# Kernel tuning notes

Hardware: AMD Instinct MI355X
Metric: run time of the kernel (lower is better)

## Reference

```python
import jax, jax.numpy as jnp
import numpy as np

N_NODES = 100000
N_EDGES = 1600000
IN = 128
OUT = 32
HEADS = 4
NEG_SLOPE = 0.2


def setup_inputs() -> dict:
    key = jax.random.key(0)
    ks = jax.random.split(key, 6)
    x = jax.random.normal(ks[0], (N_NODES, IN), dtype=jnp.float32)
    row = jax.random.randint(ks[1], (N_EDGES,), 0, N_NODES, dtype=jnp.int32)
    col = jax.random.randint(ks[2], (N_EDGES,), 0, N_NODES, dtype=jnp.int32)
    W = jax.random.normal(ks[3], (OUT * HEADS, IN), dtype=jnp.float32) * (1.0 / np.sqrt(IN))
    b = jnp.zeros((OUT * HEADS,), dtype=jnp.float32)
    a_l = jax.random.normal(ks[4], (1, OUT, HEADS), dtype=jnp.float32) * 0.1
    a_r = jax.random.normal(ks[5], (1, OUT, HEADS), dtype=jnp.float32) * 0.1
    return {"x": x, "row": row, "col": col, "W": W, "b": b, "a_l": a_l, "a_r": a_r}


def reference(x, row, col, W, b, a_l, a_r):
    N = x.shape[0]
    # Z: [N, OUT, HEADS] (row-major view of [N, OUT*HEADS], matching torch .view)
    Z = (x @ W.T + b).reshape(N, OUT, HEADS)
    e_l = jnp.sum(Z * a_l, axis=1)  # [N, HEADS]
    e_r = jnp.sum(Z * a_r, axis=1)  # [N, HEADS]
    e = e_l[row] + e_r[col]         # [E, HEADS]
    e = jnp.where(e > 0, e, NEG_SLOPE * e)  # LeakyReLU
    # segment softmax over edges grouped by destination (row)
    m = jax.ops.segment_max(e, row, num_segments=N)      # [N, HEADS]
    ex = jnp.exp(e - m[row])                              # [E, HEADS]
    denom = jax.ops.segment_sum(ex, row, num_segments=N)  # [N, HEADS]
    alpha = ex / denom[row]                               # [E, HEADS]
    # bspmm: out[i,:,h] = sum_{(i,j) in E} alpha[e,h] * Z[j,:,h]
    out = jax.ops.segment_sum(alpha[:, None, :] * Z[col], row, num_segments=N)
    return out
```

## Files before the change

### kernel.cpp

```cpp
#include <hip/hip_runtime.h>
#include <hip/hip_bf16.h>
#include <math.h>


typedef __attribute__((ext_vector_type(8))) short bf16x8;
typedef __attribute__((ext_vector_type(4))) float f32x4;

__device__ __forceinline__ ushort f2bf(float f) {
  __hip_bfloat16 h = __float2bfloat16(f);
  return __builtin_bit_cast(ushort, h);
}
__device__ __forceinline__ float bf2f(ushort u) {
  unsigned v = ((unsigned)u) << 16;
  return __builtin_bit_cast(float, v);
}

__global__ __launch_bounds__(256, 2) void gemm_deg(
    const float* __restrict__ x, const float* __restrict__ W,
    const float* __restrict__ bias, ushort* __restrict__ Zh, int N,
    const int* __restrict__ row, int* __restrict__ deg,
    int* __restrict__ rank, int E, int G1) {
  __shared__ ushort xh[64 * 128];
  __shared__ ushort xl[64 * 128];

  if ((int)blockIdx.x >= G1) {
    int e = ((int)blockIdx.x - G1) * 256 + threadIdx.x;
    if (e < E) rank[e] = atomicAdd(&deg[row[e]], 1);
    return;
  }

  const int t = threadIdx.x;
  const int lane = t & 63;
  const int wv = t >> 6;
  const int row0 = blockIdx.x * 64;
  const int l15 = lane & 15, l4 = lane >> 4;

  bf16x8 Bh[2][4], Bl[2][4];
#pragma unroll
  for (int ct = 0; ct < 2; ++ct) {
    int ch = wv * 32 + ct * 16 + l15;
#pragma unroll
    for (int kf = 0; kf < 4; ++kf) {
      int k0 = kf * 32 + l4 * 8;
      const float* wp = W + (size_t)ch * 128 + k0;
      float4 w0 = *(const float4*)(wp);
      float4 w1 = *(const float4*)(wp + 4);
      float wf[8] = {w0.x, w0.y, w0.z, w0.w, w1.x, w1.y, w1.z, w1.w};
      bf16x8 hi, lo;
#pragma unroll
      for (int j = 0; j < 8; ++j) {
        ushort hb = f2bf(wf[j]);
        hi[j] = (short)hb;
        lo[j] = (short)f2bf(wf[j] - bf2f(hb));
      }
      Bh[ct][kf] = hi;
      Bl[ct][kf] = lo;
    }
  }

#pragma unroll
  for (int i = 0; i < 8; ++i) {
    int f4 = i * 256 + t;
    int r = f4 >> 5;
    int k = (f4 & 31) * 4;
    int gr = row0 + r;
    float4 v = make_float4(0.f, 0.f, 0.f, 0.f);
    if (gr < N) v = ((const float4*)x)[(size_t)gr * 32 + (f4 & 31)];
    float vf[4] = {v.x, v.y, v.z, v.w};
    ushort hs[4], ls[4];
#pragma unroll
    for (int j = 0; j < 4; ++j) {
      hs[j] = f2bf(vf[j]);
      ls[j] = f2bf(vf[j] - bf2f(hs[j]));
    }
    int idx = r * 128 + (k ^ ((r & 7) << 3));
    uint2 hv, lv;
    hv.x = hs[0] | ((unsigned)hs[1] << 16);
    hv.y = hs[2] | ((unsigned)hs[3] << 16);
    lv.x = ls[0] | ((unsigned)ls[1] << 16);
    lv.y = ls[2] | ((unsigned)ls[3] << 16);
    *(uint2*)&xh[idx] = hv;
    *(uint2*)&xl[idx] = lv;
  }
  __syncthreads();

  f32x4 acc[4][2];
#pragma unroll
  for (int rt = 0; rt < 4; ++rt)
#pragma unroll
    for (int ct = 0; ct < 2; ++ct) acc[rt][ct] = (f32x4){0.f, 0.f, 0.f, 0.f};

#pragma unroll
  for (int kf = 0; kf < 4; ++kf) {
#pragma unroll
    for (int rt = 0; rt < 4; ++rt) {
      int r = rt * 16 + l15;
      int k = kf * 32 + l4 * 8;
      int idx = r * 128 + (k ^ ((r & 7) << 3));
      bf16x8 ah = *(const bf16x8*)&xh[idx];
      bf16x8 al = *(const bf16x8*)&xl[idx];
#pragma unroll
      for (int ct = 0; ct < 2; ++ct) {
        acc[rt][ct] = __builtin_amdgcn_mfma_f32_16x16x32_bf16(ah, Bh[ct][kf], acc[rt][ct], 0, 0, 0);
        acc[rt][ct] = __builtin_amdgcn_mfma_f32_16x16x32_bf16(al, Bh[ct][kf], acc[rt][ct], 0, 0, 0);
        acc[rt][ct] = __builtin_amdgcn_mfma_f32_16x16x32_bf16(ah, Bl[ct][kf], acc[rt][ct], 0, 0, 0);
      }
    }
  }

  float bv[2];
  bv[0] = bias[wv * 32 + l15];
  bv[1] = bias[wv * 32 + 16 + l15];
#pragma unroll
  for (int rt = 0; rt < 4; ++rt) {
#pragma unroll
    for (int ct = 0; ct < 2; ++ct) {
      int ch = wv * 32 + ct * 16 + l15;
      unsigned zc = (unsigned)((ch & 3) * 32 + (ch >> 2));
#pragma unroll
      for (int j = 0; j < 4; ++j) {
        int r = row0 + rt * 16 + l4 * 4 + j;
        if (r < N) {
          float v = acc[rt][ct][j] + bv[ct];
          Zh[(unsigned)r * 128 + zc] = f2bf(v);
        }
      }
    }
  }
}

__global__ __launch_bounds__(256) void node_scan(
    const ushort* __restrict__ Zh, const float* __restrict__ a_l,
    const float* __restrict__ a_r, float* __restrict__ el,
    float* __restrict__ er, int N4,
    const int* __restrict__ deg, int* __restrict__ basev,
    int* __restrict__ bsum, int N, int G1) {
  __shared__ float sal[128], sar[128];
  __shared__ int ss[256];
  int t = threadIdx.x;

  if ((int)blockIdx.x < G1) {
    if (t < 128) { sal[t] = a_l[t]; sar[t] = a_r[t]; }
    __syncthreads();
    int idx = blockIdx.x * 256 + t;
    if (idx >= N4) return;
    int n = idx >> 2, h = idx & 3;
    const ushort* zp = Zh + (unsigned)n * 128 + h * 32;
    float sl = 0.f, sr = 0.f;
#pragma unroll
    for (int q = 0; q < 8; ++q) {
      uint2 zz = *(const uint2*)&zp[q * 4];
      float z0 = bf2f((ushort)(zz.x & 0xffff));
      float z1 = bf2f((ushort)(zz.x >> 16));
      float z2 = bf2f((ushort)(zz.y & 0xffff));
      float z3 = bf2f((ushort)(zz.y >> 16));
      int o = q * 4;
      sl += z0 * sal[(o + 0) * 4 + h] + z1 * sal[(o + 1) * 4 + h]
          + z2 * sal[(o + 2) * 4 + h] + z3 * sal[(o + 3) * 4 + h];
      sr += z0 * sar[(o + 0) * 4 + h] + z1 * sar[(o + 1) * 4 + h]
          + z2 * sar[(o + 2) * 4 + h] + z3 * sar[(o + 3) * 4 + h];
    }
    el[idx] = sl;
    er[idx] = sr;
  } else {
    int bid = (int)blockIdx.x - G1;
    int i = bid * 256 + t;
    int v = (i < N) ? deg[i] : 0;
    ss[t] = v;
    __syncthreads();
#pragma unroll
    for (int off = 1; off < 256; off <<= 1) {
      int u = (t >= off) ? ss[t - off] : 0;
      __syncthreads();
      ss[t] += u;
      __syncthreads();
    }
    if (i < N) basev[i] = ss[t] - v;
    if (t == 255) bsum[bid] = ss[255];
  }
}

__global__ __launch_bounds__(512) void scan2(int* __restrict__ bsum, int NB) {
  __shared__ int s[512];
  int v = (threadIdx.x < NB) ? bsum[threadIdx.x] : 0;
  s[threadIdx.x] = v;
  __syncthreads();
#pragma unroll
  for (int off = 1; off < 512; off <<= 1) {
    int t = (threadIdx.x >= off) ? s[threadIdx.x - off] : 0;
    __syncthreads();
    s[threadIdx.x] += t;
    __syncthreads();
  }
  if (threadIdx.x < NB) bsum[threadIdx.x] = s[threadIdx.x] - v;
}

__global__ __launch_bounds__(256) void fill(
    const int* __restrict__ row, const int* __restrict__ col,
    const int* __restrict__ rank, const int* __restrict__ base,
    const int* __restrict__ bsum, int* __restrict__ sorted_col, int E) {
  int e = blockIdx.x * 256 + threadIdx.x;
  if (e < E) {
    int r = row[e];
    sorted_col[base[r] + bsum[r >> 8] + rank[e]] = col[e];
  }
}

__global__ __launch_bounds__(256) void gather(
    const int* __restrict__ base, const int* __restrict__ bsum,
    const int* __restrict__ deg, const int* __restrict__ sorted_col,
    const float* __restrict__ el, const float* __restrict__ er,
    const ushort* __restrict__ Zh, float* __restrict__ out, int N) {
  int t = threadIdx.x;
  int lane = t & 63;
  int n = blockIdx.x * 4 + (t >> 6);
  if (n >= N) return;
  int h = lane >> 4;
  int j = lane & 15;
  int s = base[n] + bsum[n >> 8];
  int d = deg[n];
  int end = s + d;
  float elv = el[((unsigned)n << 2) + h];
  float acc0 = 0.f, acc1 = 0.f, sumA = 0.f;
  const unsigned* Zh32 = (const unsigned*)Zh;
  const unsigned zlane = (unsigned)lane;
  const int bpb = (lane & 48) << 2;

  for (int p = s; p < end; p += 16) {
    int cnt = end - p;
    int cl6 = 0;
    float xv = 0.f;
    if (j < cnt) {
      int cl = sorted_col[p + j];
      float e = elv + er[((unsigned)cl << 2) + h];
      e = fmaxf(e, 0.2f * e);
      xv = __expf(e);
      cl6 = cl << 6;
    }
    sumA += xv;
    float xvb[16];
    unsigned addr[16];
#pragma unroll
    for (int jj = 0; jj < 16; ++jj) {
      int a = bpb + (jj << 2);
      xvb[jj] = __builtin_bit_cast(float,
          __builtin_amdgcn_ds_bpermute(a, __builtin_bit_cast(int, xv)));
      addr[jj] = (unsigned)__builtin_amdgcn_ds_bpermute(a, cl6) + zlane;
    }
    unsigned zz[16];
#pragma unroll
    for (int jj = 0; jj < 16; ++jj) zz[jj] = Zh32[addr[jj]];
#pragma unroll
    for (int jj = 0; jj < 16; ++jj) {
      acc0 = fmaf(xvb[jj], __builtin_bit_cast(float, zz[jj] << 16), acc0);
      acc1 = fmaf(xvb[jj], __builtin_bit_cast(float, zz[jj] & 0xffff0000u), acc1);
    }
  }
  float sum = sumA;
  sum += __shfl_xor(sum, 1, 64);
  sum += __shfl_xor(sum, 2, 64);
  sum += __shfl_xor(sum, 4, 64);
  sum += __shfl_xor(sum, 8, 64);
  float inv = (d > 0) ? 1.0f / sum : 0.f;
  unsigned o0 = (unsigned)(j << 1);
  unsigned ob = ((unsigned)n << 7) + (o0 << 2) + (unsigned)h;
  out[ob] = acc0 * inv;
  out[ob + 4] = acc1 * inv;
}

extern "C" void kernel_launch(void* const* d_in, const int* in_sizes, int n_in,
                              void* d_out, int out_size, void* d_ws, size_t ws_size,
                              hipStream_t stream) {
  const float* x   = (const float*)d_in[0];
  const int*   row = (const int*)d_in[1];
  const int*   col = (const int*)d_in[2];
  const float* W   = (const float*)d_in[3];
  const float* b   = (const float*)d_in[4];
  const float* a_l = (const float*)d_in[5];
  const float* a_r = (const float*)d_in[6];
  float* out = (float*)d_out;

  const int N = in_sizes[0] / 128;
  const int E = in_sizes[1];
  const int NB = (N + 255) / 256;

  char* w = (char*)d_ws;
  ushort* Zh       = (ushort*)w;             w += (size_t)N * 128 * 2;
  int*   sorted_col= (int*)w;                w += (size_t)E * 4;
  int*   rank      = (int*)w;                w += (size_t)E * 4;
  float* el        = (float*)w;              w += (size_t)N * 4 * 4;
  float* er        = (float*)w;              w += (size_t)N * 4 * 4;
  int*   deg       = (int*)w;                w += (size_t)N * 4;
  int*   base      = (int*)w;                w += (size_t)N * 4;
  int*   bsum      = (int*)w;                w += 512 * 4;

  hipMemsetAsync(deg, 0, (size_t)N * sizeof(int), stream);

  const int G1g = (N + 63) / 64;
  const int G2d = (E + 255) / 256;
  gemm_deg<<<G1g + G2d, 256, 0, stream>>>(x, W, b, Zh, N, row, deg, rank, E, G1g);

  const int G1n = (N * 4 + 255) / 256;
  node_scan<<<G1n + NB, 256, 0, stream>>>(Zh, a_l, a_r, el, er, N * 4,
                                          deg, base, bsum, N, G1n);
  scan2<<<1, 512, 0, stream>>>(bsum, NB);
  fill<<<(E + 255) / 256, 256, 0, stream>>>(row, col, rank, base, bsum,
                                            sorted_col, E);
  gather<<<(N + 3) / 4, 256, 0, stream>>>(base, bsum, deg, sorted_col, el, er,
                                          Zh, out, N);
}
```

Before: 208.9 us.

## Split fused gemm/degree kernel, precompute bf16 weight splits, use 512-thread GEMM blocks

Precomputes the hi/lo bf16 split of W once in a small prep kernel instead of in every GEMM block. The degree-counting atomics move from the fused gemm_deg launch into their own kernel. The GEMM now runs 8 waves per block, each handling 16 output channels, so per-thread accumulator and B-fragment registers are halved and occupancy can rise. This adds two kernel launches and drops the overlap the fused launch gave between atomics and the GEMM.

```diff
diff --git a/kernel.cpp b/kernel.cpp
--- a/kernel.cpp
+++ b/kernel.cpp
@@ -15,52 +15,40 @@
   return __builtin_bit_cast(float, v);
 }
 
-__global__ __launch_bounds__(256, 2) void gemm_deg(
-    const float* __restrict__ x, const float* __restrict__ W,
-    const float* __restrict__ bias, ushort* __restrict__ Zh, int N,
-    const int* __restrict__ row, int* __restrict__ deg,
-    int* __restrict__ rank, int E, int G1) {
+__global__ __launch_bounds__(256) void prep_w(
+    const float* __restrict__ W, ushort* __restrict__ Wh,
+    ushort* __restrict__ Wl) {
+  int i = blockIdx.x * 256 + threadIdx.x;
+  float w = W[i];
+  ushort hb = f2bf(w);
+  Wh[i] = hb;
+  Wl[i] = f2bf(w - bf2f(hb));
+}
+
+__global__ __launch_bounds__(512, 4) void gemm_z(
+    const float* __restrict__ x, const ushort* __restrict__ Wh,
+    const ushort* __restrict__ Wl, const float* __restrict__ bias,
+    ushort* __restrict__ Zh, int N) {
   __shared__ ushort xh[64 * 128];
   __shared__ ushort xl[64 * 128];
-
-  if ((int)blockIdx.x >= G1) {
-    int e = ((int)blockIdx.x - G1) * 256 + threadIdx.x;
-    if (e < E) rank[e] = atomicAdd(&deg[row[e]], 1);
-    return;
-  }
-
   const int t = threadIdx.x;
   const int lane = t & 63;
   const int wv = t >> 6;
   const int row0 = blockIdx.x * 64;
   const int l15 = lane & 15, l4 = lane >> 4;
-
-  bf16x8 Bh[2][4], Bl[2][4];
-#pragma unroll
-  for (int ct = 0; ct < 2; ++ct) {
-    int ch = wv * 32 + ct * 16 + l15;
-#pragma unroll
-    for (int kf = 0; kf < 4; ++kf) {
-      int k0 = kf * 32 + l4 * 8;
-      const float* wp = W + (size_t)ch * 128 + k0;
-      float4 w0 = *(const float4*)(wp);
-      float4 w1 = *(const float4*)(wp + 4);
-      float wf[8] = {w0.x, w0.y, w0.z, w0.w, w1.x, w1.y, w1.z, w1.w};
-      bf16x8 hi, lo;
-#pragma unroll
-      for (int j = 0; j < 8; ++j) {
-        ushort hb = f2bf(wf[j]);
-        hi[j] = (short)hb;
-        lo[j] = (short)f2bf(wf[j] - bf2f(hb));
-      }
-      Bh[ct][kf] = hi;
-      Bl[ct][kf] = lo;
-    }
-  }
-
-#pragma unroll
-  for (int i = 0; i < 8; ++i) {
-    int f4 = i * 256 + t;
+  const int ch = wv * 16 + l15;
+
+  bf16x8 Bh[4], Bl[4];
+#pragma unroll
+  for (int kf = 0; kf < 4; ++kf) {
+    int off = ch * 128 + kf * 32 + l4 * 8;
+    Bh[kf] = *(const bf16x8*)&Wh[off];
+    Bl[kf] = *(const bf16x8*)&Wl[off];
+  }
+
+#pragma unroll
+  for (int i = 0; i < 4; ++i) {
+    int f4 = i * 512 + t;
     int r = f4 >> 5;
     int k = (f4 & 31) * 4;
     int gr = row0 + r;
@@ -84,49 +72,41 @@
   }
   __syncthreads();
 
-  f32x4 acc[4][2];
-#pragma unroll
-  for (int rt = 0; rt < 4; ++rt)
-#pragma unroll
-    for (int ct = 0; ct < 2; ++ct) acc[rt][ct] = (f32x4){0.f, 0.f, 0.f, 0.f};
+  f32x4 acc[4];
+#pragma unroll
+  for (int rt = 0; rt < 4; ++rt) acc[rt] = (f32x4){0.f, 0.f, 0.f, 0.f};
 
 #pragma unroll
   for (int kf = 0; kf < 4; ++kf) {
 #pragma unroll
     for (int rt = 0; rt < 4; ++rt) {
       int r = rt * 16 + l15;
-      int k = kf * 32 + l4 * 8;
-      int idx = r * 128 + (k ^ ((r & 7) << 3));
+      int idx = r * 128 + ((kf * 32 + l4 * 8) ^ ((r & 7) << 3));
       bf16x8 ah = *(const bf16x8*)&xh[idx];
       bf16x8 al = *(const bf16x8*)&xl[idx];
-#pragma unroll
-      for (int ct = 0; ct < 2; ++ct) {
-        acc[rt][ct] = __builtin_amdgcn_mfma_f32_16x16x32_bf16(ah, Bh[ct][kf], acc[rt][ct], 0, 0, 0);
-        acc[rt][ct] = __builtin_amdgcn_mfma_f32_16x16x32_bf16(al, Bh[ct][kf], acc[rt][ct], 0, 0, 0);
-        acc[rt][ct] = __builtin_amdgcn_mfma_f32_16x16x32_bf16(ah, Bl[ct][kf], acc[rt][ct], 0, 0, 0);
-      }
-    }
-  }
-
-  float bv[2];
-  bv[0] = bias[wv * 32 + l15];
-  bv[1] = bias[wv * 32 + 16 + l15];
+      acc[rt] = __builtin_amdgcn_mfma_f32_16x16x32_bf16(ah, Bh[kf], acc[rt], 0, 0, 0);
+      acc[rt] = __builtin_amdgcn_mfma_f32_16x16x32_bf16(al, Bh[kf], acc[rt], 0, 0, 0);
+      acc[rt] = __builtin_amdgcn_mfma_f32_16x16x32_bf16(ah, Bl[kf], acc[rt], 0, 0, 0);
+    }
+  }
+
+  float bv = bias[ch];
+  unsigned zc = (unsigned)((ch & 3) * 32 + (ch >> 2));
 #pragma unroll
   for (int rt = 0; rt < 4; ++rt) {
 #pragma unroll
-    for (int ct = 0; ct < 2; ++ct) {
-      int ch = wv * 32 + ct * 16 + l15;
-      unsigned zc = (unsigned)((ch & 3) * 32 + (ch >> 2));
-#pragma unroll
-      for (int j = 0; j < 4; ++j) {
-        int r = row0 + rt * 16 + l4 * 4 + j;
-        if (r < N) {
-          float v = acc[rt][ct][j] + bv[ct];
-          Zh[(unsigned)r * 128 + zc] = f2bf(v);
-        }
-      }
-    }
-  }
+    for (int j = 0; j < 4; ++j) {
+      int r = row0 + rt * 16 + l4 * 4 + j;
+      if (r < N) Zh[(unsigned)r * 128 + zc] = f2bf(acc[rt][j] + bv);
+    }
+  }
+}
+
+__global__ __launch_bounds__(256) void deg_cnt(
+    const int* __restrict__ row, int* __restrict__ deg,
+    int* __restrict__ rank, int E) {
+  int e = blockIdx.x * 256 + threadIdx.x;
+  if (e < E) rank[e] = atomicAdd(&deg[row[e]], 1);
 }
 
 __global__ __launch_bounds__(256) void node_scan(
@@ -293,12 +273,14 @@
   int*   deg       = (int*)w;                w += (size_t)N * 4;
   int*   base      = (int*)w;                w += (size_t)N * 4;
   int*   bsum      = (int*)w;                w += 512 * 4;
+  ushort* Wh       = (ushort*)w;             w += 16384 * 2;
+  ushort* Wl       = (ushort*)w;             w += 16384 * 2;
 
   hipMemsetAsync(deg, 0, (size_t)N * sizeof(int), stream);
 
-  const int G1g = (N + 63) / 64;
-  const int G2d = (E + 255) / 256;
-  gemm_deg<<<G1g + G2d, 256, 0, stream>>>(x, W, b, Zh, N, row, deg, rank, E, G1g);
+  prep_w<<<64, 256, 0, stream>>>(W, Wh, Wl);
+  deg_cnt<<<(E + 255) / 256, 256, 0, stream>>>(row, deg, rank, E);
+  gemm_z<<<(N + 63) / 64, 512, 0, stream>>>(x, Wh, Wl, b, Zh, N);
 
   const int G1n = (N * 4 + 255) / 256;
   node_scan<<<G1n + NB, 256, 0, stream>>>(Zh, a_l, a_r, el, er, N * 4,
```

New measurement: 220.2 us. 1.05x slower.
